# Kernel optimization log

Hardware: AMD Instinct MI355X
Metric: run time of the kernel (lower is better)

Reference implementation:

```python
import jax, jax.numpy as jnp
import numpy as np

TEMP = 0.07  # module hardcodes self.temp = 0.07 regardless of ctor arg
N, C = 8192, 256


def setup_inputs() -> dict:
    key = jax.random.key(0)
    kq, kk = jax.random.split(key)
    q = jax.random.normal(kq, (N, C), dtype=jnp.float32)
    k = jax.random.normal(kk, (N, C), dtype=jnp.float32)
    return {"q": q, "k": k}


def reference(q, k):
    # Original builds logits = [l_pos, l_neg_row] per sample i where
    # l_pos = q_i . k_i and l_neg_row = q_i . k_j for j != i, then applies
    # CrossEntropyLoss with label 0. That logits row is exactly a permutation
    # of the full similarity row sim[i, :] = q_i @ k.T (diagonal = positive),
    # so CE(logits/T, 0) == logsumexp(sim_i/T) - sim_ii/T. Single fused GEMM
    # + row-wise logsumexp, identical math and gradients.
    sim = jnp.matmul(q, k.T) / TEMP            # [N, N]
    pos = jnp.diagonal(sim)                    # [N]
    lse = jax.nn.logsumexp(sim, axis=1)        # [N]
    return jnp.mean(lse - pos)                 # scalar loss
```

## Files before the change

kernel.cpp:

```cpp
#include <hip/hip_runtime.h>
#include <stdint.h>


#define N_ROWS 8192
#define C_DIM  256
#define BM     64
#define BN     64
#define SPLIT  8
#define JCOLS  (N_ROWS / SPLIT)
#define JTILES (JCOLS / BN)

typedef __attribute__((ext_vector_type(8))) _Float16 half8;
typedef __attribute__((ext_vector_type(4))) _Float16 half4;
typedef __attribute__((ext_vector_type(4))) float    f32x4;

#if __has_builtin(__builtin_amdgcn_exp2f)
#define EXP2(x) __builtin_amdgcn_exp2f(x)
#else
#define EXP2(x) exp2f(x)
#endif
#if __has_builtin(__builtin_amdgcn_logf)
#define LOG2(x) __builtin_amdgcn_logf(x)
#else
#define LOG2(x) log2f(x)
#endif

__device__ __forceinline__ void gload_lds16(const void* g, void* l) {
  __builtin_amdgcn_global_load_lds(
      (const __attribute__((address_space(1))) unsigned int*)g,
      (__attribute__((address_space(3))) unsigned int*)l, 16, 0, 0);
}

__global__ void cvt_kernel(const float* __restrict__ q, const float* __restrict__ k,
                           _Float16* __restrict__ qh, _Float16* __restrict__ kh) {
  const float QS = 20.60992915555663f;
  int i = blockIdx.x * 256 + threadIdx.x;
  float4 qv = ((const float4*)q)[i];
  float4 kv = ((const float4*)k)[i];
  half4 qo, ko;
  qo[0] = (_Float16)(qv.x * QS); qo[1] = (_Float16)(qv.y * QS);
  qo[2] = (_Float16)(qv.z * QS); qo[3] = (_Float16)(qv.w * QS);
  ko[0] = (_Float16)kv.x; ko[1] = (_Float16)kv.y;
  ko[2] = (_Float16)kv.z; ko[3] = (_Float16)kv.w;
  ((half4*)qh)[i] = qo;
  ((half4*)kh)[i] = ko;
}

__launch_bounds__(256, 4)
__global__ void sim_lse_kernel(const _Float16* __restrict__ qh,
                               const _Float16* __restrict__ kh,
                               float* __restrict__ pM,
                               float* __restrict__ pS,
                               float* __restrict__ pP) {
  __shared__ __align__(16) _Float16 kt[BN * C_DIM];
  const int tid  = threadIdx.x;
  const int lane = tid & 63;
  const int wave = tid >> 6;
  const int l15  = lane & 15;
  const int lg   = lane >> 4;

  const int rb   = blockIdx.x;
  const int sp   = blockIdx.y;
  const int row0 = rb * BM + wave * 16;

  half8 afrag[8];
  {
    const _Float16* qr = qh + (size_t)(row0 + l15) * C_DIM + lg * 8;
#pragma unroll
    for (int f = 0; f < 8; ++f)
      afrag[f] = *(const half8*)(qr + f * 32);
  }

  float M[4], S[4], P[4];
#pragma unroll
  for (int r = 0; r < 4; ++r) { M[r] = -__builtin_inff(); S[r] = 0.f; P[r] = -__builtin_inff(); }

  int bbase[4];
#pragma unroll
  for (int cf = 0; cf < 4; ++cf) {
    int nl = cf * 16 + l15;
    bbase[cf] = nl * 512 + (((nl & 31) * 16) ^ (lg * 16));
  }

  const char* ksrc = (const char*)(kh + (size_t)sp * JCOLS * C_DIM);
  char* lds = (char*)kt;

  for (int jt = 0; jt < JTILES; ++jt) {
    const char* src = ksrc + (size_t)jt * (BN * C_DIM * 2);
#pragma unroll
    for (int it = 0; it < 8; ++it) {
      int linear = it * 4096 + tid * 16;
      int row = linear >> 9;
      int c16 = (linear >> 4) & 31;
      int gc  = c16 ^ (row & 31);
      gload_lds16(src + row * 512 + gc * 16, lds + linear);
    }
    __syncthreads();

    f32x4 acc[4];
#pragma unroll
    for (int cf = 0; cf < 4; ++cf) { f32x4 z = {0.f, 0.f, 0.f, 0.f}; acc[cf] = z; }

#pragma unroll
    for (int ks = 0; ks < 8; ++ks) {
#pragma unroll
      for (int cf = 0; cf < 4; ++cf) {
        half8 b = *(const half8*)(lds + (bbase[cf] ^ (ks * 64)));
        acc[cf] = __builtin_amdgcn_mfma_f32_16x16x32_f16(afrag[ks], b, acc[cf], 0, 0, 0);
      }
    }
    __syncthreads();

    const int j0 = sp * JCOLS + jt * BN;

    if (row0 >= j0 && row0 < j0 + BN) {
#pragma unroll
      for (int r = 0; r < 4; ++r) {
        int d = row0 - j0 + lg * 4 + r;
#pragma unroll
        for (int cf = 0; cf < 4; ++cf)
          if (cf * 16 + l15 == d) P[r] = acc[cf][r];
      }
    }

#pragma unroll
    for (int r = 0; r < 4; ++r) {
      float v0 = acc[0][r], v1 = acc[1][r], v2 = acc[2][r], v3 = acc[3][r];
      float tmax = fmaxf(fmaxf(v0, v1), fmaxf(v2, v3));
      float newM  = fmaxf(M[r], tmax);
      float alpha = EXP2(M[r] - newM);
      float p = EXP2(v0 - newM) + EXP2(v1 - newM) +
                EXP2(v2 - newM) + EXP2(v3 - newM);
      S[r] = fmaf(S[r], alpha, p);
      M[r] = newM;
    }
  }

#pragma unroll
  for (int r = 0; r < 4; ++r) {
#pragma unroll
    for (int off = 1; off < 16; off <<= 1) {
      float Mo = __shfl_xor(M[r], off);
      float So = __shfl_xor(S[r], off);
      float nm = fmaxf(M[r], Mo);
      S[r] = S[r] * EXP2(M[r] - nm) + So * EXP2(Mo - nm);
      M[r] = nm;
      P[r] = fmaxf(P[r], __shfl_xor(P[r], off));
    }
  }

  if (l15 == 0) {
#pragma unroll
    for (int r = 0; r < 4; ++r) {
      int grow = row0 + lg * 4 + r;
      pM[(size_t)sp * N_ROWS + grow] = M[r];
      pS[(size_t)sp * N_ROWS + grow] = S[r];
      pP[(size_t)sp * N_ROWS + grow] = P[r];
    }
  }
}

__global__ void finish1_kernel(const float* __restrict__ pM, const float* __restrict__ pS,
                               const float* __restrict__ pP, float* __restrict__ pPart) {
  const int tid = threadIdx.x;
  const int r = blockIdx.x * 256 + tid;
  float m = -__builtin_inff();
#pragma unroll
  for (int s = 0; s < SPLIT; ++s) m = fmaxf(m, pM[s * N_ROWS + r]);
  float ssum = 0.f;
  float pos  = -__builtin_inff();
#pragma unroll
  for (int s = 0; s < SPLIT; ++s) {
    ssum = fmaf(pS[s * N_ROWS + r], EXP2(pM[s * N_ROWS + r] - m), ssum);
    pos = fmaxf(pos, pP[s * N_ROWS + r]);
  }
  float accl = (m + LOG2(ssum)) - pos;
#pragma unroll
  for (int off = 1; off < 64; off <<= 1) accl += __shfl_xor(accl, off);
  __shared__ float wsum[4];
  if ((tid & 63) == 0) wsum[tid >> 6] = accl;
  __syncthreads();
  if (tid == 0)
    pPart[blockIdx.x] = wsum[0] + wsum[1] + wsum[2] + wsum[3];
}

__global__ void finish2_kernel(const float* __restrict__ pPart, float* __restrict__ out) {
  const int tid = threadIdx.x;
  float v = (tid < 32) ? pPart[tid] : 0.f;
#pragma unroll
  for (int off = 1; off < 64; off <<= 1) v += __shfl_xor(v, off);
  if (tid == 0)
    out[0] = v * (0.69314718055994531f / (float)N_ROWS);
}

extern "C" void kernel_launch(void* const* d_in, const int* in_sizes, int n_in,
                              void* d_out, int out_size, void* d_ws, size_t ws_size,
                              hipStream_t stream) {
  const float* q = (const float*)d_in[0];
  const float* k = (const float*)d_in[1];
  float* out = (float*)d_out;
  char* ws = (char*)d_ws;

  _Float16* qh = (_Float16*)ws;
  _Float16* kh = (_Float16*)(ws + (size_t)N_ROWS * C_DIM * 2);
  float* pM = (float*)(ws + (size_t)N_ROWS * C_DIM * 4);
  float* pS = pM + SPLIT * N_ROWS;
  float* pP = pS + SPLIT * N_ROWS;
  float* pPart = pP + SPLIT * N_ROWS;

  cvt_kernel<<<dim3(N_ROWS * C_DIM / 4 / 256), dim3(256), 0, stream>>>(q, k, qh, kh);
  sim_lse_kernel<<<dim3(N_ROWS / BM, SPLIT), dim3(256), 0, stream>>>(qh, kh, pM, pS, pP);
  finish1_kernel<<<dim3(N_ROWS / 256), dim3(256), 0, stream>>>(pM, pS, pP, pPart);
  finish2_kernel<<<dim3(1), dim3(64), 0, stream>>>(pPart, out);
}
```

Baseline: 110.6 us.

## Enlarge row tile, double-buffer K tiles, compute diagonal in convert kernel

Each wave now keeps four 16-row Q fragments in registers, so every K fragment read from LDS feeds four MFMAs instead of one. This cuts LDS traffic per FLOP. The K tile is double-buffered so the next tile's global-to-LDS load overlaps the current tile's compute, and SPLIT is raised to keep enough blocks in the grid. The diagonal positive logit is now computed in the convert kernel with a wave reduction over each row, which removes per-tile diagonal checks. The cost is more registers per thread and twice the LDS per block, with occupancy dropping to 2 blocks per CU.

```diff
diff --git a/kernel.cpp b/kernel.cpp
--- a/kernel.cpp
+++ b/kernel.cpp
@@ -4,11 +4,12 @@
 
 #define N_ROWS 8192
 #define C_DIM  256
-#define BM     64
 #define BN     64
-#define SPLIT  8
+#define SPLIT  16
 #define JCOLS  (N_ROWS / SPLIT)
 #define JTILES (JCOLS / BN)
+#define RF     4
+#define BLK_ROWS 256
 
 typedef __attribute__((ext_vector_type(8))) _Float16 half8;
 typedef __attribute__((ext_vector_type(4))) _Float16 half4;
@@ -32,7 +33,8 @@
 }
 
 __global__ void cvt_kernel(const float* __restrict__ q, const float* __restrict__ k,
-                           _Float16* __restrict__ qh, _Float16* __restrict__ kh) {
+                           _Float16* __restrict__ qh, _Float16* __restrict__ kh,
+                           float* __restrict__ pP) {
   const float QS = 20.60992915555663f;
   int i = blockIdx.x * 256 + threadIdx.x;
   float4 qv = ((const float4*)q)[i];
@@ -44,15 +46,22 @@
   ko[2] = (_Float16)kv.z; ko[3] = (_Float16)kv.w;
   ((half4*)qh)[i] = qo;
   ((half4*)kh)[i] = ko;
-}
-
-__launch_bounds__(256, 4)
+
+  float d = (float)qo[0] * (float)ko[0];
+  d = fmaf((float)qo[1], (float)ko[1], d);
+  d = fmaf((float)qo[2], (float)ko[2], d);
+  d = fmaf((float)qo[3], (float)ko[3], d);
+#pragma unroll
+  for (int off = 1; off < 64; off <<= 1) d += __shfl_xor(d, off);
+  if ((threadIdx.x & 63) == 0) pP[i >> 6] = d;
+}
+
+__launch_bounds__(256, 2)
 __global__ void sim_lse_kernel(const _Float16* __restrict__ qh,
                                const _Float16* __restrict__ kh,
                                float* __restrict__ pM,
-                               float* __restrict__ pS,
-                               float* __restrict__ pP) {
-  __shared__ __align__(16) _Float16 kt[BN * C_DIM];
+                               float* __restrict__ pS) {
+  __shared__ __align__(16) _Float16 kt[2 * BN * C_DIM];
   const int tid  = threadIdx.x;
   const int lane = tid & 63;
   const int wave = tid >> 6;
@@ -61,19 +70,21 @@
 
   const int rb   = blockIdx.x;
   const int sp   = blockIdx.y;
-  const int row0 = rb * BM + wave * 16;
-
-  half8 afrag[8];
-  {
-    const _Float16* qr = qh + (size_t)(row0 + l15) * C_DIM + lg * 8;
-#pragma unroll
-    for (int f = 0; f < 8; ++f)
-      afrag[f] = *(const half8*)(qr + f * 32);
-  }
-
-  float M[4], S[4], P[4];
-#pragma unroll
-  for (int r = 0; r < 4; ++r) { M[r] = -__builtin_inff(); S[r] = 0.f; P[r] = -__builtin_inff(); }
+  const int row0 = rb * BLK_ROWS + wave * 64;
+
+  half8 a[RF][8];
+#pragma unroll
+  for (int rf = 0; rf < RF; ++rf) {
+    const _Float16* qr = qh + (size_t)(row0 + rf * 16 + l15) * C_DIM + lg * 8;
+#pragma unroll
+    for (int f = 0; f < 8; ++f) a[rf][f] = *(const half8*)(qr + f * 32);
+  }
+
+  float M[RF][4], S[RF][4];
+#pragma unroll
+  for (int rf = 0; rf < RF; ++rf)
+#pragma unroll
+    for (int r = 0; r < 4; ++r) { M[rf][r] = -__builtin_inff(); S[rf][r] = 0.f; }
 
   int bbase[4];
 #pragma unroll
@@ -85,78 +96,89 @@
   const char* ksrc = (const char*)(kh + (size_t)sp * JCOLS * C_DIM);
   char* lds = (char*)kt;
 
+#pragma unroll
+  for (int it = 0; it < 8; ++it) {
+    int linear = it * 4096 + tid * 16;
+    int row = linear >> 9;
+    int gc  = ((linear >> 4) & 31) ^ (row & 31);
+    gload_lds16(ksrc + row * 512 + gc * 16, lds + linear);
+  }
+
+#pragma unroll 2
   for (int jt = 0; jt < JTILES; ++jt) {
-    const char* src = ksrc + (size_t)jt * (BN * C_DIM * 2);
-#pragma unroll
-    for (int it = 0; it < 8; ++it) {
-      int linear = it * 4096 + tid * 16;
-      int row = linear >> 9;
-      int c16 = (linear >> 4) & 31;
-      int gc  = c16 ^ (row & 31);
-      gload_lds16(src + row * 512 + gc * 16, lds + linear);
+    __syncthreads();
+    const char* cur = lds + (jt & 1) * 32768;
+
+    if (jt + 1 < JTILES) {
+      const char* src = ksrc + (size_t)(jt + 1) * (BN * C_DIM * 2);
+      char* nxt = lds + ((jt + 1) & 1) * 32768;
+#pragma unroll
+      for (int it = 0; it < 8; ++it) {
+        int linear = it * 4096 + tid * 16;
+        int row = linear >> 9;
+        int gc  = ((linear >> 4) & 31) ^ (row & 31);
+        gload_lds16(src + row * 512 + gc * 16, nxt + linear);
+      }
     }
-    __syncthreads();
-
-    f32x4 acc[4];
-#pragma unroll
-    for (int cf = 0; cf < 4; ++cf) { f32x4 z = {0.f, 0.f, 0.f, 0.f}; acc[cf] = z; }
-
-#pragma unroll
-    for (int ks = 0; ks < 8; ++ks) {
-#pragma unroll
-      for (int cf = 0; cf < 4; ++cf) {
-        half8 b = *(const half8*)(lds + (bbase[cf] ^ (ks * 64)));
-        acc[cf] = __builtin_amdgcn_mfma_f32_16x16x32_f16(afrag[ks], b, acc[cf], 0, 0, 0);
-      }
+
+#pragma unroll
+    for (int cp = 0; cp < 2; ++cp) {
+      f32x4 acc0[RF], acc1[RF];
+#pragma unroll
+      for (int rf = 0; rf < RF; ++rf) {
+        f32x4 z = {0.f, 0.f, 0.f, 0.f};
+        acc0[rf] = z; acc1[rf] = z;
+      }
+      const int b0off = bbase[cp * 2];
+      const int b1off = bbase[cp * 2 + 1];
+#pragma unroll
+      for (int ks = 0; ks < 8; ++ks) {
+        half8 b0 = *(const half8*)(cur + (b0off ^ (ks * 64)));
+        half8 b1 = *(const half8*)(cur + (b1off ^ (ks * 64)));
+#pragma unroll
+        for (int rf = 0; rf < RF; ++rf) {
+          acc0[rf] = __builtin_amdgcn_mfma_f32_16x16x32_f16(a[rf][ks], b0, acc0[rf], 0, 0, 0);
+          acc1[rf] = __builtin_amdgcn_mfma_f32_16x16x32_f16(a[rf][ks], b1, acc1[rf], 0, 0, 0);
+        }
+      }
+#pragma unroll
+      for (int rf = 0; rf < RF; ++rf)
+#pragma unroll
+        for (int r = 0; r < 4; ++r) {
+          float v0 = acc0[rf][r], v1 = acc1[rf][r];
+          float tmax  = fmaxf(v0, v1);
+          float newM  = fmaxf(M[rf][r], tmax);
+          float alpha = EXP2(M[rf][r] - newM);
+          float p = EXP2(v0 - newM) + EXP2(v1 - newM);
+          S[rf][r] = fmaf(S[rf][r], alpha, p);
+          M[rf][r] = newM;
+        }
     }
-    __syncthreads();
-
-    const int j0 = sp * JCOLS + jt * BN;
-
-    if (row0 >= j0 && row0 < j0 + BN) {
+  }
+
+#pragma unroll
+  for (int rf = 0; rf < RF; ++rf)
+#pragma unroll
+    for (int r = 0; r < 4; ++r) {
+#pragma unroll
+      for (int off = 1; off < 16; off <<= 1) {
+        float Mo = __shfl_xor(M[rf][r], off);
+        float So = __shfl_xor(S[rf][r], off);
+        float nm = fmaxf(M[rf][r], Mo);
+        S[rf][r] = S[rf][r] * EXP2(M[rf][r] - nm) + So * EXP2(Mo - nm);
+        M[rf][r] = nm;
+      }
+    }
+
+  if (l15 == 0) {
+#pragma unroll
+    for (int rf = 0; rf < RF; ++rf)
 #pragma unroll
       for (int r = 0; r < 4; ++r) {
-        int d = row0 - j0 + lg * 4 + r;
-#pragma unroll
-        for (int cf = 0; cf < 4; ++cf)
-          if (cf * 16 + l15 == d) P[r] = acc[cf][r];
-      }
-    }
-
-#pragma unroll
-    for (int r = 0; r < 4; ++r) {
-      float v0 = acc[0][r], v1 = acc[1][r], v2 = acc[2][r], v3 = acc[3][r];
-      float tmax = fmaxf(fmaxf(v0, v1), fmaxf(v2, v3));
-      float newM  = fmaxf(M[r], tmax);
-      float alpha = EXP2(M[r] - newM);
-      float p = EXP2(v0 - newM) + EXP2(v1 - newM) +
-                EXP2(v2 - newM) + EXP2(v3 - newM);
-      S[r] = fmaf(S[r], alpha, p);
-      M[r] = newM;
-    }
-  }
-
-#pragma unroll
-  for (int r = 0; r < 4; ++r) {
-#pragma unroll
-    for (int off = 1; off < 16; off <<= 1) {
-      float Mo = __shfl_xor(M[r], off);
-      float So = __shfl_xor(S[r], off);
-      float nm = fmaxf(M[r], Mo);
-      S[r] = S[r] * EXP2(M[r] - nm) + So * EXP2(Mo - nm);
-      M[r] = nm;
-      P[r] = fmaxf(P[r], __shfl_xor(P[r], off));
-    }
-  }
-
-  if (l15 == 0) {
-#pragma unroll
-    for (int r = 0; r < 4; ++r) {
-      int grow = row0 + lg * 4 + r;
-      pM[(size_t)sp * N_ROWS + grow] = M[r];
-      pS[(size_t)sp * N_ROWS + grow] = S[r];
-      pP[(size_t)sp * N_ROWS + grow] = P[r];
-    }
+        int grow = row0 + rf * 16 + lg * 4 + r;
+        pM[(size_t)sp * N_ROWS + grow] = M[rf][r];
+        pS[(size_t)sp * N_ROWS + grow] = S[rf][r];
+      }
   }
 }
 
@@ -168,13 +190,10 @@
 #pragma unroll
   for (int s = 0; s < SPLIT; ++s) m = fmaxf(m, pM[s * N_ROWS + r]);
   float ssum = 0.f;
-  float pos  = -__builtin_inff();
-#pragma unroll
-  for (int s = 0; s < SPLIT; ++s) {
+#pragma unroll
+  for (int s = 0; s < SPLIT; ++s)
     ssum = fmaf(pS[s * N_ROWS + r], EXP2(pM[s * N_ROWS + r] - m), ssum);
-    pos = fmaxf(pos, pP[s * N_ROWS + r]);
-  }
-  float accl = (m + LOG2(ssum)) - pos;
+  float accl = (m + LOG2(ssum)) - pP[r];
 #pragma unroll
   for (int off = 1; off < 64; off <<= 1) accl += __shfl_xor(accl, off);
   __shared__ float wsum[4];
@@ -206,10 +225,10 @@
   float* pM = (float*)(ws + (size_t)N_ROWS * C_DIM * 4);
   float* pS = pM + SPLIT * N_ROWS;
   float* pP = pS + SPLIT * N_ROWS;
-  float* pPart = pP + SPLIT * N_ROWS;
-
-  cvt_kernel<<<dim3(N_ROWS * C_DIM / 4 / 256), dim3(256), 0, stream>>>(q, k, qh, kh);
-  sim_lse_kernel<<<dim3(N_ROWS / BM, SPLIT), dim3(256), 0, stream>>>(qh, kh, pM, pS, pP);
+  float* pPart = pP + N_ROWS;
+
+  cvt_kernel<<<dim3(N_ROWS * C_DIM / 4 / 256), dim3(256), 0, stream>>>(q, k, qh, kh, pP);
+  sim_lse_kernel<<<dim3(N_ROWS / BLK_ROWS, SPLIT), dim3(256), 0, stream>>>(qh, kh, pM, pS);
   finish1_kernel<<<dim3(N_ROWS / 256), dim3(256), 0, stream>>>(pM, pS, pP, pPart);
   finish2_kernel<<<dim3(1), dim3(64), 0, stream>>>(pPart, out);
 }
```

After: 137.9 us. 24.7% more time.
